# Performance work log

Hardware: AMD Instinct MI355X
Metric: run time of the kernel (lower is better)

The kernel has to match this reference:

```python
import jax, jax.numpy as jnp
import numpy as np

E = 1024   # embed_dim
H = 16     # num_heads
D = E // H # head_dim
NP = 2     # n_physics
PH = 16    # physics adapter hidden


def setup_inputs() -> dict:
    key = jax.random.key(0)
    ks = jax.random.split(key, 16)
    B, T = 2, 2048
    s = 0.02
    return {
        "x": jax.random.normal(ks[0], (B, T, E), dtype=jnp.float32),
        "physics_state": jax.random.uniform(ks[1], (B, NP), dtype=jnp.float32),
        "attn_mask": jax.random.randint(ks[2], (B, T), 0, 2).astype(jnp.bool_),
        "Wq": jax.random.normal(ks[3], (E, E), dtype=jnp.float32) * s,
        "bq": jnp.zeros((E,), dtype=jnp.float32),
        "Wk": jax.random.normal(ks[4], (E, E), dtype=jnp.float32) * s,
        "bk": jnp.zeros((E,), dtype=jnp.float32),
        "Wv": jax.random.normal(ks[5], (E, E), dtype=jnp.float32) * s,
        "bv": jnp.zeros((E,), dtype=jnp.float32),
        "Wo": jax.random.normal(ks[6], (E, E), dtype=jnp.float32) * s,
        "bo": jnp.zeros((E,), dtype=jnp.float32),
        "Wp1": jax.random.normal(ks[7], (NP, PH), dtype=jnp.float32) * 0.5,
        "bp1": jnp.zeros((PH,), dtype=jnp.float32),
        "Wp2": jax.random.normal(ks[8], (PH, H), dtype=jnp.float32) * 0.25,
        "bp2": jnp.zeros((H,), dtype=jnp.float32),
    }


def reference(x, physics_state, attn_mask, Wq, bq, Wk, bk, Wv, bv, Wo, bo, Wp1, bp1, Wp2, bp2):
    B, T, _ = x.shape
    scale = 1.0 / np.sqrt(D)
    # projections -> (B, H, T, D)
    q = (x @ Wq + bq).reshape(B, T, H, D).transpose(0, 2, 1, 3)
    k = (x @ Wk + bk).reshape(B, T, H, D).transpose(0, 2, 1, 3)
    v = (x @ Wv + bv).reshape(B, T, H, D).transpose(0, 2, 1, 3)
    # per-head physics bias (B, H) -> (B, H, 1, 1)
    h = jax.nn.gelu(physics_state @ Wp1 + bp1, approximate=False)
    phys_bias = (h @ Wp2 + bp2)[:, :, None, None]
    scores = jnp.einsum("bhqd,bhkd->bhqk", q, k) * scale + phys_bias
    # key padding mask: True = keep
    scores = jnp.where(attn_mask[:, None, None, :], scores, -jnp.inf)
    attn = jax.nn.softmax(scores, axis=-1)
    out = jnp.einsum("bhqk,bhkd->bhqd", attn, v)
    out = out.transpose(0, 2, 1, 3).reshape(B, T, E)
    return out @ Wo + bo
```

## Files before the change

### kernel.cpp

```cpp
#include <hip/hip_runtime.h>
#include <hip/hip_bf16.h>
#include <stdint.h>

#define E_  1024
#define H_  16
#define D_  64
#define T_  2048
#define B_  2

typedef unsigned short u16;
typedef unsigned char u8;
typedef __attribute__((ext_vector_type(8))) __bf16 bf16x8;
typedef __attribute__((ext_vector_type(4))) float f32x4;
typedef __attribute__((ext_vector_type(8))) u16 u16x8;
typedef __attribute__((ext_vector_type(4))) u16 u16x4;

__device__ __forceinline__ float bf2f(u16 u) {
  union { uint32_t u32; float f; } x; x.u32 = ((uint32_t)u) << 16; return x.f;
}
__device__ __forceinline__ u16 f2bf(float v) {
  union { float f; uint32_t u; } x; x.f = v;
  uint32_t r = x.u + 0x7fffu + ((x.u >> 16) & 1u);
  return (u16)(r >> 16);
}
__device__ __forceinline__ void async16(const void* g, void* l) {
  __builtin_amdgcn_global_load_lds(
      (const __attribute__((address_space(1))) void*)g,
      (__attribute__((address_space(3))) void*)l, 16, 0, 0);
}
__device__ __forceinline__ int jperm(int k) {
  return (k & 35) | ((k & 12) << 1) | ((k & 16) >> 2);
}

__device__ __forceinline__ int detect_f32(const void* src) {
  u16 u = ((const u16*)src)[2 * (threadIdx.x & 63)];
  int e = (u >> 7) & 0xFF;
  int ex = (e != 0 && (e <= 0x40 || e >= 0xC0)) ? 1 : 0;
  return __popcll(__ballot(ex)) > 16;
}

__global__ __launch_bounds__(256) void convf_kernel(const void* __restrict__ src,
                                                    u16* __restrict__ dst, int n) {
  const int f32in = detect_f32(src);
  int i = (blockIdx.x * 256 + threadIdx.x) * 8;
  if (i >= n) return;
  if (f32in) {
    const float* s = (const float*)src;
    u16x8 o;
#pragma unroll
    for (int j = 0; j < 8; ++j) o[j] = f2bf(s[i + j]);
    *(u16x8*)(dst + i) = o;
  } else {
    *(u16x8*)(dst + i) = *(const u16x8*)((const u16*)src + i);
  }
}

__global__ __launch_bounds__(256) void bias4_kernel(
    const void* __restrict__ b0, const void* __restrict__ b1,
    const void* __restrict__ b2, const void* __restrict__ b3,
    u16* __restrict__ dst) {
  const void* src = (blockIdx.x == 0) ? b0 : (blockIdx.x == 1) ? b1
                    : (blockIdx.x == 2) ? b2 : b3;
  const int f32in = detect_f32(src);
  u16* d = dst + blockIdx.x * 2048;
  int t = threadIdx.x;
#pragma unroll
  for (int j = 0; j < 4; ++j) {
    int i = t + j * 256;
    d[i] = f32in ? f2bf(((const float*)src)[i]) : ((const u16*)src)[i];
  }
}

__global__ __launch_bounds__(256) void maskbias_kernel(const void* __restrict__ mp,
                                                       float* __restrict__ mbg) {
  unsigned w0 = ((const unsigned*)mp)[threadIdx.x & 63];
  int isInt = (__ballot(w0 > 1u) == 0ull);
  int i = blockIdx.x * 256 + threadIdx.x;
  int keep = isInt ? (((const int*)mp)[i] != 0) : (((const u8*)mp)[i] != 0);
  mbg[i] = keep ? -5.77078016f : -30000.f;
}

__global__ __launch_bounds__(256) void wtc4_kernel(
    const void* __restrict__ W0, const void* __restrict__ W1,
    const void* __restrict__ W2, const void* __restrict__ W3,
    u16* __restrict__ T0, u16* __restrict__ T1,
    u16* __restrict__ T2, u16* __restrict__ T3) {
  __shared__ __align__(16) u16 tile[64][65];
  const int z = blockIdx.z;
  const void* Wv = (z == 0) ? W0 : (z == 1) ? W1 : (z == 2) ? W2 : W3;
  u16* WT = (z == 0) ? T0 : (z == 1) ? T1 : (z == 2) ? T2 : T3;
  const int f32in = detect_f32(Wv);
  const int bx = blockIdx.x * 64, by = blockIdx.y * 64;
  const int t = threadIdx.x;
#pragma unroll
  for (int p = 0; p < 2; ++p) {
    int row = p * 32 + (t >> 3);
    int ch = t & 7;
    if (f32in) {
      const float* s = (const float*)Wv + (size_t)(by + row) * E_ + bx + ch * 8;
#pragma unroll
      for (int j = 0; j < 8; ++j) tile[row][ch * 8 + j] = f2bf(s[j]);
    } else {
      u16x8 v = *(const u16x8*)((const u16*)Wv + (size_t)(by + row) * E_ + bx + ch * 8);
#pragma unroll
      for (int j = 0; j < 8; ++j) tile[row][ch * 8 + j] = v[j];
    }
  }
  __syncthreads();
#pragma unroll
  for (int p = 0; p < 2; ++p) {
    int orow = p * 32 + (t >> 3);
    int ch = t & 7;
    u16x8 v;
#pragma unroll
    for (int j = 0; j < 8; ++j) v[j] = tile[ch * 8 + j][orow];
    *(u16x8*)(WT + (size_t)(bx + orow) * E_ + by + ch * 8) = v;
  }
}

__global__ __launch_bounds__(256, 2) void gemm_qkv_kernel(
    const u16* __restrict__ A, const u16* __restrict__ BTm,
    const u16* __restrict__ biases, u16* __restrict__ Qb,
    u16* __restrict__ Kb, u16* __restrict__ Vtb) {
  __shared__ __align__(16) u16 As[128 * 64];
  __shared__ __align__(16) u16 Bs[128 * 64];
  const int tid = threadIdx.x, lane = tid & 63, wid = tid >> 6;
  const int wm = wid >> 1, wn = wid & 1;
  const int l15 = lane & 15, lg = lane >> 4;
  const int r0 = blockIdx.x * 128, c0 = blockIdx.y * 128;
  f32x4 acc[4][4] = {};

  for (int k0 = 0; k0 < E_; k0 += 64) {
    __syncthreads();
#pragma unroll
    for (int i = 0; i < 4; ++i) {
      int row = i * 32 + (tid >> 3);
      int g = (tid & 7) ^ (row & 7);
      async16(A + (size_t)(r0 + row) * E_ + k0 + g * 8,
              (char*)As + i * 4096 + tid * 16);
      async16(BTm + (size_t)(c0 + row) * E_ + k0 + g * 8,
              (char*)Bs + i * 4096 + tid * 16);
    }
    __syncthreads();
#pragma unroll
    for (int kk = 0; kk < 2; ++kk) {
      bf16x8 af[4], bfr[4];
#pragma unroll
      for (int mt = 0; mt < 4; ++mt) {
        int rowa = wm * 64 + mt * 16 + l15;
        int sa = (kk * 4 + lg) ^ (rowa & 7);
        af[mt] = *(const bf16x8*)((const char*)As + rowa * 128 + sa * 16);
        int rowb = wn * 64 + mt * 16 + l15;
        int sb = (kk * 4 + lg) ^ (rowb & 7);
        bfr[mt] = *(const bf16x8*)((const char*)Bs + rowb * 128 + sb * 16);
      }
#pragma unroll
      for (int mt = 0; mt < 4; ++mt)
#pragma unroll
        for (int nt = 0; nt < 4; ++nt)
          acc[mt][nt] = __builtin_amdgcn_mfma_f32_16x16x32_bf16(
              af[mt], bfr[nt], acc[mt][nt], 0, 0, 0);
    }
  }

  const int sel = c0 >> 10;
  u16* outp = (sel == 0) ? Qb : Kb;
#pragma unroll
  for (int mt = 0; mt < 4; ++mt) {
#pragma unroll
    for (int nt = 0; nt < 4; ++nt) {
      int colG = c0 + wn * 64 + nt * 16 + l15;
      int colL = colG & 1023;
      float bv = bf2f(biases[sel * 2048 + colL]);
      int rbase = r0 + wm * 64 + mt * 16 + lg * 4;
      int hh = colL >> 6, dd = colL & 63;
      if (sel == 2) {
        int bb = rbase >> 11, t0 = rbase & (T_ - 1);
        int tp = (t0 & ~63) | jperm(t0 & 63);
        u16x4 pk;
#pragma unroll
        for (int r = 0; r < 4; ++r) pk[r] = f2bf(acc[mt][nt][r] + bv);
        *(u16x4*)(Vtb + (size_t)((bb * H_ + hh) * D_ + dd) * T_ + tp) = pk;
      } else {
#pragma unroll
        for (int r = 0; r < 4; ++r) {
          int row = rbase + r;
          int bb = row >> 11, t = row & (T_ - 1);
          outp[(size_t)((bb * H_ + hh) * T_ + t) * D_ + dd] =
              f2bf(acc[mt][nt][r] + bv);
        }
      }
    }
  }
}

__global__ __launch_bounds__(256, 2) void gemm_out_kernel(
    const u16* __restrict__ A, const u16* __restrict__ BTm,
    const u16* __restrict__ bias, float* __restrict__ out) {
  __shared__ __align__(16) u16 As[128 * 64];
  __shared__ __align__(16) u16 Bs[128 * 64];
  const int tid = threadIdx.x, lane = tid & 63, wid = tid >> 6;
  const int wm = wid >> 1, wn = wid & 1;
  const int l15 = lane & 15, lg = lane >> 4;
  const int r0 = blockIdx.x * 128, c0 = blockIdx.y * 128;
  f32x4 acc[4][4] = {};

  for (int k0 = 0; k0 < E_; k0 += 64) {
    __syncthreads();
#pragma unroll
    for (int i = 0; i < 4; ++i) {
      int row = i * 32 + (tid >> 3);
      int g = (tid & 7) ^ (row & 7);
      async16(A + (size_t)(r0 + row) * E_ + k0 + g * 8,
              (char*)As + i * 4096 + tid * 16);
      async16(BTm + (size_t)(c0 + row) * E_ + k0 + g * 8,
              (char*)Bs + i * 4096 + tid * 16);
    }
    __syncthreads();
#pragma unroll
    for (int kk = 0; kk < 2; ++kk) {
      bf16x8 af[4], bfr[4];
#pragma unroll
      for (int mt = 0; mt < 4; ++mt) {
        int rowa = wm * 64 + mt * 16 + l15;
        int sa = (kk * 4 + lg) ^ (rowa & 7);
        af[mt] = *(const bf16x8*)((const char*)As + rowa * 128 + sa * 16);
        int rowb = wn * 64 + mt * 16 + l15;
        int sb = (kk * 4 + lg) ^ (rowb & 7);
        bfr[mt] = *(const bf16x8*)((const char*)Bs + rowb * 128 + sb * 16);
      }
#pragma unroll
      for (int mt = 0; mt < 4; ++mt)
#pragma unroll
        for (int nt = 0; nt < 4; ++nt)
          acc[mt][nt] = __builtin_amdgcn_mfma_f32_16x16x32_bf16(
              af[mt], bfr[nt], acc[mt][nt], 0, 0, 0);
    }
  }

#pragma unroll
  for (int mt = 0; mt < 4; ++mt)
#pragma unroll
    for (int nt = 0; nt < 4; ++nt) {
      int col = c0 + wn * 64 + nt * 16 + l15;
      float bv = bf2f(bias[col]);
      int rbase = r0 + wm * 64 + mt * 16 + lg * 4;
#pragma unroll
      for (int r = 0; r < 4; ++r)
        out[(size_t)(rbase + r) * E_ + col] = acc[mt][nt][r] + bv;
    }
}

__global__ __launch_bounds__(256, 2) void attn_kernel(
    const u16* __restrict__ Q, const u16* __restrict__ K,
    const u16* __restrict__ VT, const float* __restrict__ mbg,
    u16* __restrict__ outb) {
  __shared__ __align__(16) u16 Ks[2][64 * 64];
  __shared__ __align__(16) u16 Vs[2][64 * 64];
  const int wg = blockIdx.x;
  const int xcd = wg & 7, slot = wg >> 3;
  const int bh = xcd + 8 * (slot >> 4);
  const int q0 = (slot & 15) * 128;
  const int b = bh >> 4, h = bh & 15;
  const int tid = threadIdx.x, lane = tid & 63, w = tid >> 6;
  const int l15 = lane & 15, lg = lane >> 4;

  const u16* qb = Q + (size_t)bh * T_ * D_;
  const u16* kb = K + (size_t)bh * T_ * D_;
  const u16* vb = VT + (size_t)bh * D_ * T_;
  const float* mbb = mbg + b * T_ + lg * 4;

  bf16x8 qf[2][2];
#pragma unroll
  for (int mt = 0; mt < 2; ++mt)
#pragma unroll
    for (int kd = 0; kd < 2; ++kd) {
      int row = q0 + w * 32 + mt * 16 + l15;
      qf[mt][kd] = *(const bf16x8*)(qb + (size_t)row * D_ + kd * 32 + lg * 8);
    }

#define STAGE(kt_, bi_)                                                  \
  do {                                                                   \
    _Pragma("unroll")                                                    \
    for (int c = 0; c < 2; ++c) {                                        \
      int row_ = c * 32 + (tid >> 3);                                    \
      int g_ = (tid & 7) ^ (row_ & 7);                                   \
      async16(kb + (size_t)((kt_) * 64 + row_) * D_ + g_ * 8,            \
              (char*)&Ks[bi_][0] + c * 4096 + tid * 16);                 \
      async16(vb + (size_t)row_ * T_ + (kt_) * 64 + g_ * 8,              \
              (char*)&Vs[bi_][0] + c * 4096 + tid * 16);                 \
    }                                                                    \
  } while (0)

  STAGE(0, 0);
  __syncthreads();

  f32x4 o[2][4] = {};
  float lrow[2] = {0.f, 0.f};
  const float cc = 0.125f * 1.44269504f;

  for (int kt = 0; kt < 32; ++kt) {
    const int cur = kt & 1;
    if (kt < 31) STAGE(kt + 1, cur ^ 1);
    const char* Kc = (const char*)&Ks[cur][0];
    const char* Vc = (const char*)&Vs[cur][0];

    f32x4 mbv4[4];
#pragma unroll
    for (int mf = 0; mf < 4; ++mf)
      mbv4[mf] = *(const f32x4*)(mbb + kt * 64 + mf * 16);

    f32x4 s2[2][4] = {};
#pragma unroll
    for (int kd = 0; kd < 2; ++kd) {
      bf16x8 kf[4];
#pragma unroll
      for (int mf = 0; mf < 4; ++mf) {
        int row = mf * 16 + l15;
        int sl = (kd * 4 + lg) ^ (row & 7);
        kf[mf] = *(const bf16x8*)(Kc + row * 128 + sl * 16);
      }
      __builtin_amdgcn_s_setprio(1);
#pragma unroll
      for (int mt = 0; mt < 2; ++mt)
#pragma unroll
        for (int mf = 0; mf < 4; ++mf)
          s2[mt][mf] = __builtin_amdgcn_mfma_f32_16x16x32_bf16(
              kf[mf], qf[mt][kd], s2[mt][mf], 0, 0, 0);
      __builtin_amdgcn_s_setprio(0);
    }

    uint32_t pkw[2][4][2];
#pragma unroll
    for (int mt = 0; mt < 2; ++mt) {
#pragma unroll
      for (int mf = 0; mf < 4; ++mf) {
        float p0 = exp2f(fmaf(s2[mt][mf][0], cc, mbv4[mf][0]));
        float p1 = exp2f(fmaf(s2[mt][mf][1], cc, mbv4[mf][1]));
        float p2 = exp2f(fmaf(s2[mt][mf][2], cc, mbv4[mf][2]));
        float p3 = exp2f(fmaf(s2[mt][mf][3], cc, mbv4[mf][3]));
        lrow[mt] += (p0 + p1) + (p2 + p3);
        asm("v_cvt_pk_bf16_f32 %0, %1, %2" : "=v"(pkw[mt][mf][0]) : "v"(p0), "v"(p1));
        asm("v_cvt_pk_bf16_f32 %0, %1, %2" : "=v"(pkw[mt][mf][1]) : "v"(p2), "v"(p3));
      }
    }

#pragma unroll
    for (int kk = 0; kk < 2; ++kk) {
      bf16x8 pf[2], vf[4];
#pragma unroll
      for (int mt = 0; mt < 2; ++mt) {
        union { uint32_t u[4]; bf16x8 v; } pu;
        pu.u[0] = pkw[mt][2 * kk][0];
        pu.u[1] = pkw[mt][2 * kk][1];
        pu.u[2] = pkw[mt][2 * kk + 1][0];
        pu.u[3] = pkw[mt][2 * kk + 1][1];
        pf[mt] = pu.v;
      }
#pragma unroll
      for (int df = 0; df < 4; ++df) {
        int row = df * 16 + l15;
        int sl = (kk * 4 + lg) ^ (row & 7);
        vf[df] = *(const bf16x8*)(Vc + row * 128 + sl * 16);
      }
      __builtin_amdgcn_s_setprio(1);
#pragma unroll
      for (int mt = 0; mt < 2; ++mt)
#pragma unroll
        for (int df = 0; df < 4; ++df)
          o[mt][df] = __builtin_amdgcn_mfma_f32_16x16x32_bf16(
              pf[mt], vf[df], o[mt][df], 0, 0, 0);
      __builtin_amdgcn_s_setprio(0);
    }
    __syncthreads();
  }
#undef STAGE

  float inv[2][4];
#pragma unroll
  for (int mt = 0; mt < 2; ++mt) {
    float t = lrow[mt];
    t += __shfl_xor(t, 16);
    t += __shfl_xor(t, 32);
    float ti = (t > 0.f) ? 1.0f / t : 0.f;
#pragma unroll
    for (int r = 0; r < 4; ++r)
      inv[mt][r] = __shfl(ti, (lane & 48) | (lg * 4 + r));
  }

  char* wbase = ((w < 2) ? (char*)&Ks[0][0] : (char*)&Vs[0][0]) + (w & 1) * 4608;
#pragma unroll
  for (int mt = 0; mt < 2; ++mt)
#pragma unroll
    for (int df = 0; df < 4; ++df)
#pragma unroll
      for (int r = 0; r < 4; ++r) {
        int prow = mt * 16 + lg * 4 + r;
        *(u16*)(wbase + prow * 144 + (df * 16 + l15) * 2) =
            f2bf(o[mt][df][r] * inv[mt][r]);
      }
  asm volatile("s_waitcnt lgkmcnt(0)" ::: "memory");
  __builtin_amdgcn_sched_barrier(0);
  {
    int rowL = lane >> 1;
    int c8 = lane & 1;
    int grow = b * T_ + q0 + w * 32 + rowL;
#pragma unroll
    for (int j = 0; j < 4; ++j) {
      int chunk = c8 + 2 * j;
      u16x8 v = *(const u16x8*)(wbase + rowL * 144 + chunk * 16);
      *(u16x8*)(outb + (size_t)grow * E_ + h * D_ + chunk * 8) = v;
    }
  }
}

extern "C" void kernel_launch(void* const* d_in, const int* in_sizes, int n_in,
                              void* d_out, int out_size, void* d_ws, size_t ws_size,
                              hipStream_t stream) {
  const void* x    = d_in[0];
  const void* mask = d_in[2];
  const void* Wq = d_in[3];
  const void* bq = d_in[4];
  const void* Wk = d_in[5];
  const void* bk = d_in[6];
  const void* Wv = d_in[7];
  const void* bv = d_in[8];
  const void* Wo = d_in[9];
  const void* bo = d_in[10];
  char* ws = (char*)d_ws;

  const size_t MB = 1024 * 1024;
  u16* Kb   = (u16*)(ws + 0 * MB);
  u16* Vtb  = (u16*)(ws + 8 * MB);
  u16* Ab   = (u16*)(ws + 16 * MB);
  u16* WqT  = (u16*)(ws + 16 * MB);
  u16* WkT  = (u16*)(ws + 18 * MB);
  u16* WvT  = (u16*)(ws + 20 * MB);
  u16* WoT  = (u16*)(ws + 24 * MB);
  u16* bqc  = (u16*)(ws + 26 * MB);
  u16* boc  = bqc + 3 * 2048;
  float* mbg = (float*)(ws + 26 * MB + 32 * 1024);

  u16* Qb = (u16*)d_out;
  u16* xc = (u16*)((char*)d_out + 8 * MB);
  float* out = (float*)d_out;

  dim3 blk(256);
  const int NX = B_ * T_ * E_;

  convf_kernel<<<NX / 8 / 256, blk, 0, stream>>>(x, xc, NX);
  bias4_kernel<<<4, blk, 0, stream>>>(bq, bk, bv, bo, bqc);
  maskbias_kernel<<<16, blk, 0, stream>>>(mask, mbg);
  wtc4_kernel<<<dim3(16, 16, 4), blk, 0, stream>>>(Wq, Wk, Wv, Wo,
                                                   WqT, WkT, WvT, WoT);
  gemm_qkv_kernel<<<dim3(32, 24), blk, 0, stream>>>(xc, WqT, bqc, Qb, Kb, Vtb);
  attn_kernel<<<dim3(512), blk, 0, stream>>>(Qb, Kb, Vtb, mbg, Ab);
  gemm_out_kernel<<<dim3(32, 8), blk, 0, stream>>>(Ab, WoT, boc, out);
}
```

Before: 129.0 us.

## Triple-buffer K/V tiles with one barrier per iteration and stage mask in LDS

Moves the attention K/V shared-memory pipeline from double to triple buffering, prefetching two tiles ahead. It replaces the two __syncthreads per iteration with a vmcnt wait plus a single s_barrier. The mask bias row is copied once into LDS instead of being read from global memory every iteration, and the output staging gets its own scratch buffer so it no longer reuses the K/V buffers. The added LDS (about 8KB mask, 18KB scratch, extra K/V stage) may reduce occupancy below the 2 blocks per CU that the launch bounds target.

```diff
diff --git a/kernel.cpp b/kernel.cpp
--- a/kernel.cpp
+++ b/kernel.cpp
@@ -255,8 +255,10 @@
     const u16* __restrict__ Q, const u16* __restrict__ K,
     const u16* __restrict__ VT, const float* __restrict__ mbg,
     u16* __restrict__ outb) {
-  __shared__ __align__(16) u16 Ks[2][64 * 64];
-  __shared__ __align__(16) u16 Vs[2][64 * 64];
+  __shared__ __align__(16) u16 Ks[3][64 * 64];
+  __shared__ __align__(16) u16 Vs[3][64 * 64];
+  __shared__ __align__(16) float mb[T_];
+  __shared__ __align__(16) u16 oscr[4][2304];
   const int wg = blockIdx.x;
   const int xcd = wg & 7, slot = wg >> 3;
   const int bh = xcd + 8 * (slot >> 4);
@@ -268,7 +270,13 @@
   const u16* qb = Q + (size_t)bh * T_ * D_;
   const u16* kb = K + (size_t)bh * T_ * D_;
   const u16* vb = VT + (size_t)bh * D_ * T_;
-  const float* mbb = mbg + b * T_ + lg * 4;
+
+  {
+    const f32x4* s = (const f32x4*)(mbg + b * T_);
+    f32x4* d = (f32x4*)mb;
+#pragma unroll
+    for (int j = 0; j < 2; ++j) d[tid + j * 256] = s[tid + j * 256];
+  }
 
   bf16x8 qf[2][2];
 #pragma unroll
@@ -293,22 +301,30 @@
   } while (0)
 
   STAGE(0, 0);
-  __syncthreads();
+  STAGE(1, 1);
+  asm volatile("s_waitcnt lgkmcnt(0)" ::: "memory");
 
   f32x4 o[2][4] = {};
   float lrow[2] = {0.f, 0.f};
   const float cc = 0.125f * 1.44269504f;
 
+  int rd = 0, wr = 2;
   for (int kt = 0; kt < 32; ++kt) {
-    const int cur = kt & 1;
-    if (kt < 31) STAGE(kt + 1, cur ^ 1);
-    const char* Kc = (const char*)&Ks[cur][0];
-    const char* Vc = (const char*)&Vs[cur][0];
+    if (kt < 31)
+      asm volatile("s_waitcnt vmcnt(4)" ::: "memory");
+    else
+      asm volatile("s_waitcnt vmcnt(0)" ::: "memory");
+    __builtin_amdgcn_sched_barrier(0);
+    __builtin_amdgcn_s_barrier();
+    __builtin_amdgcn_sched_barrier(0);
+    if (kt < 30) STAGE(kt + 2, wr);
+    const char* Kc = (const char*)&Ks[rd][0];
+    const char* Vc = (const char*)&Vs[rd][0];
 
     f32x4 mbv4[4];
 #pragma unroll
     for (int mf = 0; mf < 4; ++mf)
-      mbv4[mf] = *(const f32x4*)(mbb + kt * 64 + mf * 16);
+      mbv4[mf] = *(const f32x4*)&mb[kt * 64 + mf * 16 + lg * 4];
 
     f32x4 s2[2][4] = {};
 #pragma unroll
@@ -372,7 +388,8 @@
               pf[mt], vf[df], o[mt][df], 0, 0, 0);
       __builtin_amdgcn_s_setprio(0);
     }
-    __syncthreads();
+    rd = (rd == 2) ? 0 : rd + 1;
+    wr = (wr == 2) ? 0 : wr + 1;
   }
 #undef STAGE
 
@@ -388,7 +405,7 @@
       inv[mt][r] = __shfl(ti, (lane & 48) | (lg * 4 + r));
   }
 
-  char* wbase = ((w < 2) ? (char*)&Ks[0][0] : (char*)&Vs[0][0]) + (w & 1) * 4608;
+  char* wbase = (char*)&oscr[w][0];
 #pragma unroll
   for (int mt = 0; mt < 2; ++mt)
 #pragma unroll
```

Measured after the change: 129.3 us. Within noise of the previous version (+0.3%).

## Halve attention query tile, double grid, stage bf16 mask bias in LDS

Applied to the files above, without the earlier changes.

The attention kernel now handles 64 query rows per workgroup instead of 128, with one 16-row MFMA tile per wave, and launches 1024 workgroups with a higher occupancy hint. The mask bias is stored as bf16 and copied once into shared memory per block, so it is no longer read from global memory on every key tile. This aims to cut per-wave register pressure and raise occupancy and parallelism. In exchange, each workgroup reloads K and V for fewer queries, which doubles K/V traffic, and the bias loses some precision.

```diff
diff --git a/kernel.cpp b/kernel.cpp
--- a/kernel.cpp
+++ b/kernel.cpp
@@ -72,12 +72,12 @@
 }
 
 __global__ __launch_bounds__(256) void maskbias_kernel(const void* __restrict__ mp,
-                                                       float* __restrict__ mbg) {
+                                                       u16* __restrict__ mbh) {
   unsigned w0 = ((const unsigned*)mp)[threadIdx.x & 63];
   int isInt = (__ballot(w0 > 1u) == 0ull);
   int i = blockIdx.x * 256 + threadIdx.x;
   int keep = isInt ? (((const int*)mp)[i] != 0) : (((const u8*)mp)[i] != 0);
-  mbg[i] = keep ? -5.77078016f : -30000.f;
+  mbh[i] = keep ? f2bf(-5.77078016f) : f2bf(-30000.f);
 }
 
 __global__ __launch_bounds__(256) void wtc4_kernel(
@@ -251,16 +251,17 @@
     }
 }
 
-__global__ __launch_bounds__(256, 2) void attn_kernel(
+__global__ __launch_bounds__(256, 4) void attn_kernel(
     const u16* __restrict__ Q, const u16* __restrict__ K,
-    const u16* __restrict__ VT, const float* __restrict__ mbg,
+    const u16* __restrict__ VT, const u16* __restrict__ mbg,
     u16* __restrict__ outb) {
   __shared__ __align__(16) u16 Ks[2][64 * 64];
   __shared__ __align__(16) u16 Vs[2][64 * 64];
+  __shared__ __align__(16) u16 mbh[T_];
   const int wg = blockIdx.x;
   const int xcd = wg & 7, slot = wg >> 3;
-  const int bh = xcd + 8 * (slot >> 4);
-  const int q0 = (slot & 15) * 128;
+  const int bh = xcd + 8 * (slot >> 5);
+  const int q0 = (slot & 31) * 64;
   const int b = bh >> 4, h = bh & 15;
   const int tid = threadIdx.x, lane = tid & 63, w = tid >> 6;
   const int l15 = lane & 15, lg = lane >> 4;
@@ -268,16 +269,15 @@
   const u16* qb = Q + (size_t)bh * T_ * D_;
   const u16* kb = K + (size_t)bh * T_ * D_;
   const u16* vb = VT + (size_t)bh * D_ * T_;
-  const float* mbb = mbg + b * T_ + lg * 4;
-
-  bf16x8 qf[2][2];
-#pragma unroll
-  for (int mt = 0; mt < 2; ++mt)
-#pragma unroll
-    for (int kd = 0; kd < 2; ++kd) {
-      int row = q0 + w * 32 + mt * 16 + l15;
-      qf[mt][kd] = *(const bf16x8*)(qb + (size_t)row * D_ + kd * 32 + lg * 8);
-    }
+
+  *(u16x8*)&mbh[tid * 8] = *(const u16x8*)(mbg + b * T_ + tid * 8);
+
+  bf16x8 qf[2];
+#pragma unroll
+  for (int kd = 0; kd < 2; ++kd) {
+    int row = q0 + w * 16 + l15;
+    qf[kd] = *(const bf16x8*)(qb + (size_t)row * D_ + kd * 32 + lg * 8);
+  }
 
 #define STAGE(kt_, bi_)                                                  \
   do {                                                                   \
@@ -295,8 +295,8 @@
   STAGE(0, 0);
   __syncthreads();
 
-  f32x4 o[2][4] = {};
-  float lrow[2] = {0.f, 0.f};
+  f32x4 o[4] = {};
+  float lrow = 0.f;
   const float cc = 0.125f * 1.44269504f;
 
   for (int kt = 0; kt < 32; ++kt) {
@@ -305,12 +305,12 @@
     const char* Kc = (const char*)&Ks[cur][0];
     const char* Vc = (const char*)&Vs[cur][0];
 
-    f32x4 mbv4[4];
+    u16x4 mraw[4];
 #pragma unroll
     for (int mf = 0; mf < 4; ++mf)
-      mbv4[mf] = *(const f32x4*)(mbb + kt * 64 + mf * 16);
-
-    f32x4 s2[2][4] = {};
+      mraw[mf] = *(const u16x4*)&mbh[kt * 64 + mf * 16 + lg * 4];
+
+    f32x4 s2[4] = {};
 #pragma unroll
     for (int kd = 0; kd < 2; ++kd) {
       bf16x8 kf[4];
@@ -322,40 +322,34 @@
       }
       __builtin_amdgcn_s_setprio(1);
 #pragma unroll
-      for (int mt = 0; mt < 2; ++mt)
-#pragma unroll
-        for (int mf = 0; mf < 4; ++mf)
-          s2[mt][mf] = __builtin_amdgcn_mfma_f32_16x16x32_bf16(
-              kf[mf], qf[mt][kd], s2[mt][mf], 0, 0, 0);
+      for (int mf = 0; mf < 4; ++mf)
+        s2[mf] = __builtin_amdgcn_mfma_f32_16x16x32_bf16(
+            kf[mf], qf[kd], s2[mf], 0, 0, 0);
       __builtin_amdgcn_s_setprio(0);
     }
 
-    uint32_t pkw[2][4][2];
-#pragma unroll
-    for (int mt = 0; mt < 2; ++mt) {
-#pragma unroll
-      for (int mf = 0; mf < 4; ++mf) {
-        float p0 = exp2f(fmaf(s2[mt][mf][0], cc, mbv4[mf][0]));
-        float p1 = exp2f(fmaf(s2[mt][mf][1], cc, mbv4[mf][1]));
-        float p2 = exp2f(fmaf(s2[mt][mf][2], cc, mbv4[mf][2]));
-        float p3 = exp2f(fmaf(s2[mt][mf][3], cc, mbv4[mf][3]));
-        lrow[mt] += (p0 + p1) + (p2 + p3);
-        asm("v_cvt_pk_bf16_f32 %0, %1, %2" : "=v"(pkw[mt][mf][0]) : "v"(p0), "v"(p1));
-        asm("v_cvt_pk_bf16_f32 %0, %1, %2" : "=v"(pkw[mt][mf][1]) : "v"(p2), "v"(p3));
-      }
+    uint32_t pkw[4][2];
+#pragma unroll
+    for (int mf = 0; mf < 4; ++mf) {
+      float p0 = exp2f(fmaf(s2[mf][0], cc, bf2f(mraw[mf][0])));
+      float p1 = exp2f(fmaf(s2[mf][1], cc, bf2f(mraw[mf][1])));
+      float p2 = exp2f(fmaf(s2[mf][2], cc, bf2f(mraw[mf][2])));
+      float p3 = exp2f(fmaf(s2[mf][3], cc, bf2f(mraw[mf][3])));
+      lrow += (p0 + p1) + (p2 + p3);
+      asm("v_cvt_pk_bf16_f32 %0, %1, %2" : "=v"(pkw[mf][0]) : "v"(p0), "v"(p1));
+      asm("v_cvt_pk_bf16_f32 %0, %1, %2" : "=v"(pkw[mf][1]) : "v"(p2), "v"(p3));
     }
 
 #pragma unroll
     for (int kk = 0; kk < 2; ++kk) {
-      bf16x8 pf[2], vf[4];
-#pragma unroll
-      for (int mt = 0; mt < 2; ++mt) {
+      bf16x8 pf, vf[4];
+      {
         union { uint32_t u[4]; bf16x8 v; } pu;
-        pu.u[0] = pkw[mt][2 * kk][0];
-        pu.u[1] = pkw[mt][2 * kk][1];
-        pu.u[2] = pkw[mt][2 * kk + 1][0];
-        pu.u[3] = pkw[mt][2 * kk + 1][1];
-        pf[mt] = pu.v;
+        pu.u[0] = pkw[2 * kk][0];
+        pu.u[1] = pkw[2 * kk][1];
+        pu.u[2] = pkw[2 * kk + 1][0];
+        pu.u[3] = pkw[2 * kk + 1][1];
+        pf = pu.v;
       }
 #pragma unroll
       for (int df = 0; df < 4; ++df) {
@@ -365,49 +359,44 @@
       }
       __builtin_amdgcn_s_setprio(1);
 #pragma unroll
-      for (int mt = 0; mt < 2; ++mt)
-#pragma unroll
-        for (int df = 0; df < 4; ++df)
-          o[mt][df] = __builtin_amdgcn_mfma_f32_16x16x32_bf16(
-              pf[mt], vf[df], o[mt][df], 0, 0, 0);
+      for (int df = 0; df < 4; ++df)
+        o[df] = __builtin_amdgcn_mfma_f32_16x16x32_bf16(
+            pf, vf[df], o[df], 0, 0, 0);
       __builtin_amdgcn_s_setprio(0);
     }
     __syncthreads();
   }
 #undef STAGE
 
-  float inv[2][4];
-#pragma unroll
-  for (int mt = 0; mt < 2; ++mt) {
-    float t = lrow[mt];
+  float inv[4];
+  {
+    float t = lrow;
     t += __shfl_xor(t, 16);
     t += __shfl_xor(t, 32);
     float ti = (t > 0.f) ? 1.0f / t : 0.f;
 #pragma unroll
     for (int r = 0; r < 4; ++r)
-      inv[mt][r] = __shfl(ti, (lane & 48) | (lg * 4 + r));
-  }
-
-  char* wbase = ((w < 2) ? (char*)&Ks[0][0] : (char*)&Vs[0][0]) + (w & 1) * 4608;
-#pragma unroll
-  for (int mt = 0; mt < 2; ++mt)
-#pragma unroll
-    for (int df = 0; df < 4; ++df)
-#pragma unroll
-      for (int r = 0; r < 4; ++r) {
-        int prow = mt * 16 + lg * 4 + r;
-        *(u16*)(wbase + prow * 144 + (df * 16 + l15) * 2) =
-            f2bf(o[mt][df][r] * inv[mt][r]);
-      }
+      inv[r] = __shfl(ti, (lane & 48) | (lg * 4 + r));
+  }
+
+  char* wbase = (char*)&Ks[0][0] + w * 2304;
+#pragma unroll
+  for (int df = 0; df < 4; ++df)
+#pragma unroll
+    for (int r = 0; r < 4; ++r) {
+      int prow = lg * 4 + r;
+      *(u16*)(wbase + prow * 144 + (df * 16 + l15) * 2) =
+          f2bf(o[df][r] * inv[r]);
+    }
   asm volatile("s_waitcnt lgkmcnt(0)" ::: "memory");
   __builtin_amdgcn_sched_barrier(0);
   {
-    int rowL = lane >> 1;
-    int c8 = lane & 1;
-    int grow = b * T_ + q0 + w * 32 + rowL;
-#pragma unroll
-    for (int j = 0; j < 4; ++j) {
-      int chunk = c8 + 2 * j;
+    int rowL = lane >> 2;
+    int cpart = lane & 3;
+    int grow = b * T_ + q0 + w * 16 + rowL;
+#pragma unroll
+    for (int j = 0; j < 2; ++j) {
+      int chunk = cpart + 4 * j;
       u16x8 v = *(const u16x8*)(wbase + rowL * 144 + chunk * 16);
       *(u16x8*)(outb + (size_t)grow * E_ + h * D_ + chunk * 8) = v;
     }
@@ -439,7 +428,7 @@
   u16* WoT  = (u16*)(ws + 24 * MB);
   u16* bqc  = (u16*)(ws + 26 * MB);
   u16* boc  = bqc + 3 * 2048;
-  float* mbg = (float*)(ws + 26 * MB + 32 * 1024);
+  u16* mbg  = (u16*)(ws + 26 * MB + 32 * 1024);
 
   u16* Qb = (u16*)d_out;
   u16* xc = (u16*)((char*)d_out + 8 * MB);
@@ -454,6 +443,6 @@
   wtc4_kernel<<<dim3(16, 16, 4), blk, 0, stream>>>(Wq, Wk, Wv, Wo,
                                                    WqT, WkT, WvT, WoT);
   gemm_qkv_kernel<<<dim3(32, 24), blk, 0, stream>>>(xc, WqT, bqc, Qb, Kb, Vtb);
-  attn_kernel<<<dim3(512), blk, 0, stream>>>(Qb, Kb, Vtb, mbg, Ab);
+  attn_kernel<<<dim3(1024), blk, 0, stream>>>(Qb, Kb, Vtb, mbg, Ab);
   gemm_out_kernel<<<dim3(32, 8), blk, 0, stream>>>(Ab, WoT, boc, out);
 }
```

After: 132.1 us. 2.4% more time.

## Software-pipeline attention: prefetch two tiles ahead and overlap PV with next QK

Applied to the files above, without the earlier changes.

Restructures the attention main loop so K/V tiles are staged two iterations ahead in a 3-way K and 4-way V LDS ring, with explicit vmcnt waits and a single barrier per tile. The PV matmul of the previous tile is interleaved after the QK matmul of the current tile, using ping-pong packed-probability registers, so MFMA work overlaps the exp/softmax VALU work. The mask bias is copied into LDS once instead of read from global every tile. GEMM launch bounds move to 3 waves per SIMD. The cost is more LDS and registers, which can reduce attention occupancy. The hand-written waitcnt accounting may also be fragile.

```diff
diff --git a/kernel.cpp b/kernel.cpp
--- a/kernel.cpp
+++ b/kernel.cpp
@@ -118,7 +118,7 @@
   }
 }
 
-__global__ __launch_bounds__(256, 2) void gemm_qkv_kernel(
+__global__ __launch_bounds__(256, 3) void gemm_qkv_kernel(
     const u16* __restrict__ A, const u16* __restrict__ BTm,
     const u16* __restrict__ biases, u16* __restrict__ Qb,
     u16* __restrict__ Kb, u16* __restrict__ Vtb) {
@@ -194,7 +194,7 @@
   }
 }
 
-__global__ __launch_bounds__(256, 2) void gemm_out_kernel(
+__global__ __launch_bounds__(256, 3) void gemm_out_kernel(
     const u16* __restrict__ A, const u16* __restrict__ BTm,
     const u16* __restrict__ bias, float* __restrict__ out) {
   __shared__ __align__(16) u16 As[128 * 64];
@@ -251,12 +251,13 @@
     }
 }
 
-__global__ __launch_bounds__(256, 2) void attn_kernel(
+__global__ __launch_bounds__(256) void attn_kernel(
     const u16* __restrict__ Q, const u16* __restrict__ K,
     const u16* __restrict__ VT, const float* __restrict__ mbg,
     u16* __restrict__ outb) {
-  __shared__ __align__(16) u16 Ks[2][64 * 64];
-  __shared__ __align__(16) u16 Vs[2][64 * 64];
+  __shared__ __align__(16) u16 Ks[3 * 64 * 64];
+  __shared__ __align__(16) u16 Vs[4 * 64 * 64];
+  __shared__ __align__(16) float mb[T_];
   const int wg = blockIdx.x;
   const int xcd = wg & 7, slot = wg >> 3;
   const int bh = xcd + 8 * (slot >> 4);
@@ -268,7 +269,13 @@
   const u16* qb = Q + (size_t)bh * T_ * D_;
   const u16* kb = K + (size_t)bh * T_ * D_;
   const u16* vb = VT + (size_t)bh * D_ * T_;
-  const float* mbb = mbg + b * T_ + lg * 4;
+
+  {
+    const f32x4* s = (const f32x4*)(mbg + b * T_);
+    f32x4* d = (f32x4*)mb;
+#pragma unroll
+    for (int j = 0; j < 2; ++j) d[tid + j * 256] = s[tid + j * 256];
+  }
 
   bf16x8 qf[2][2];
 #pragma unroll
@@ -279,102 +286,125 @@
       qf[mt][kd] = *(const bf16x8*)(qb + (size_t)row * D_ + kd * 32 + lg * 8);
     }
 
-#define STAGE(kt_, bi_)                                                  \
+#define STAGE(n_)                                                        \
   do {                                                                   \
+    char* kdst_ = (char*)Ks + ((n_) % 3) * 8192;                         \
+    char* vdst_ = (char*)Vs + ((n_) & 3) * 8192;                         \
     _Pragma("unroll")                                                    \
     for (int c = 0; c < 2; ++c) {                                        \
       int row_ = c * 32 + (tid >> 3);                                    \
       int g_ = (tid & 7) ^ (row_ & 7);                                   \
-      async16(kb + (size_t)((kt_) * 64 + row_) * D_ + g_ * 8,            \
-              (char*)&Ks[bi_][0] + c * 4096 + tid * 16);                 \
-      async16(vb + (size_t)row_ * T_ + (kt_) * 64 + g_ * 8,              \
-              (char*)&Vs[bi_][0] + c * 4096 + tid * 16);                 \
+      async16(kb + (size_t)((n_) * 64 + row_) * D_ + g_ * 8,             \
+              kdst_ + c * 4096 + tid * 16);                              \
+      async16(vb + (size_t)row_ * T_ + (n_) * 64 + g_ * 8,               \
+              vdst_ + c * 4096 + tid * 16);                              \
     }                                                                    \
   } while (0)
 
-  STAGE(0, 0);
-  __syncthreads();
+#define PVBODY(vt_, PRV)                                                 \
+  do {                                                                   \
+    const char* Vp_ = (const char*)Vs + ((vt_) & 3) * 8192;              \
+    _Pragma("unroll")                                                    \
+    for (int kk = 0; kk < 2; ++kk) {                                     \
+      bf16x8 pf[2], vf[4];                                               \
+      _Pragma("unroll")                                                  \
+      for (int mt = 0; mt < 2; ++mt) {                                   \
+        union { uint32_t u[4]; bf16x8 v; } pu;                           \
+        pu.u[0] = PRV[mt][2 * kk][0];                                    \
+        pu.u[1] = PRV[mt][2 * kk][1];                                    \
+        pu.u[2] = PRV[mt][2 * kk + 1][0];                                \
+        pu.u[3] = PRV[mt][2 * kk + 1][1];                                \
+        pf[mt] = pu.v;                                                   \
+      }                                                                  \
+      _Pragma("unroll")                                                  \
+      for (int df = 0; df < 4; ++df) {                                   \
+        int row_ = df * 16 + l15;                                        \
+        int sl_ = (kk * 4 + lg) ^ (row_ & 7);                            \
+        vf[df] = *(const bf16x8*)(Vp_ + row_ * 128 + sl_ * 16);          \
+      }                                                                  \
+      __builtin_amdgcn_s_setprio(1);                                     \
+      _Pragma("unroll")                                                  \
+      for (int mt = 0; mt < 2; ++mt)                                     \
+        _Pragma("unroll")                                                \
+        for (int df = 0; df < 4; ++df)                                   \
+          o[mt][df] = __builtin_amdgcn_mfma_f32_16x16x32_bf16(           \
+              pf[mt], vf[df], o[mt][df], 0, 0, 0);                       \
+      __builtin_amdgcn_s_setprio(0);                                     \
+    }                                                                    \
+  } while (0)
+
+#define TILE(kt_, CUR, PRV, DOPV)                                        \
+  do {                                                                   \
+    if ((kt_) < 31) asm volatile("s_waitcnt vmcnt(4)" ::: "memory");     \
+    else            asm volatile("s_waitcnt vmcnt(0)" ::: "memory");     \
+    __builtin_amdgcn_sched_barrier(0);                                   \
+    __builtin_amdgcn_s_barrier();                                        \
+    __builtin_amdgcn_sched_barrier(0);                                   \
+    if ((kt_) < 30) STAGE((kt_) + 2);                                    \
+    const char* Kc_ = (const char*)Ks + ((kt_) % 3) * 8192;              \
+    f32x4 mbv4[4];                                                       \
+    _Pragma("unroll")                                                    \
+    for (int mf = 0; mf < 4; ++mf)                                       \
+      mbv4[mf] = *(const f32x4*)&mb[(kt_) * 64 + mf * 16 + lg * 4];      \
+    f32x4 s2[2][4] = {};                                                 \
+    _Pragma("unroll")                                                    \
+    for (int kd = 0; kd < 2; ++kd) {                                     \
+      bf16x8 kf[4];                                                      \
+      _Pragma("unroll")                                                  \
+      for (int mf = 0; mf < 4; ++mf) {                                   \
+        int row_ = mf * 16 + l15;                                        \
+        int sl_ = (kd * 4 + lg) ^ (row_ & 7);                            \
+        kf[mf] = *(const bf16x8*)(Kc_ + row_ * 128 + sl_ * 16);          \
+      }                                                                  \
+      __builtin_amdgcn_s_setprio(1);                                     \
+      _Pragma("unroll")                                                  \
+      for (int mt = 0; mt < 2; ++mt)                                     \
+        _Pragma("unroll")                                                \
+        for (int mf = 0; mf < 4; ++mf)                                   \
+          s2[mt][mf] = __builtin_amdgcn_mfma_f32_16x16x32_bf16(          \
+              kf[mf], qf[mt][kd], s2[mt][mf], 0, 0, 0);                  \
+      __builtin_amdgcn_s_setprio(0);                                     \
+    }                                                                    \
+    if (DOPV) PVBODY((kt_) - 1, PRV);       \
+    _Pragma("unroll")                                                    \
+    for (int mt = 0; mt < 2; ++mt) {                                     \
+      _Pragma("unroll")                                                  \
+      for (int mf = 0; mf < 4; ++mf) {                                   \
+        float p0 = exp2f(fmaf(s2[mt][mf][0], cc, mbv4[mf][0]));          \
+        float p1 = exp2f(fmaf(s2[mt][mf][1], cc, mbv4[mf][1]));          \
+        float p2 = exp2f(fmaf(s2[mt][mf][2], cc, mbv4[mf][2]));          \
+        float p3 = exp2f(fmaf(s2[mt][mf][3], cc, mbv4[mf][3]));          \
+        lrow[mt] += (p0 + p1) + (p2 + p3);                               \
+        asm("v_cvt_pk_bf16_f32 %0, %1, %2"                               \
+            : "=v"(CUR[mt][mf][0]) : "v"(p0), "v"(p1));                  \
+        asm("v_cvt_pk_bf16_f32 %0, %1, %2"                               \
+            : "=v"(CUR[mt][mf][1]) : "v"(p2), "v"(p3));                  \
+      }                                                                  \
+    }                                                                    \
+  } while (0)
+
+  STAGE(0);
+  STAGE(1);
+  asm volatile("s_waitcnt lgkmcnt(0)" ::: "memory");
 
   f32x4 o[2][4] = {};
   float lrow[2] = {0.f, 0.f};
+  uint32_t pkwA[2][4][2], pkwB[2][4][2];
   const float cc = 0.125f * 1.44269504f;
 
-  for (int kt = 0; kt < 32; ++kt) {
-    const int cur = kt & 1;
-    if (kt < 31) STAGE(kt + 1, cur ^ 1);
-    const char* Kc = (const char*)&Ks[cur][0];
-    const char* Vc = (const char*)&Vs[cur][0];
-
-    f32x4 mbv4[4];
-#pragma unroll
-    for (int mf = 0; mf < 4; ++mf)
-      mbv4[mf] = *(const f32x4*)(mbb + kt * 64 + mf * 16);
-
-    f32x4 s2[2][4] = {};
-#pragma unroll
-    for (int kd = 0; kd < 2; ++kd) {
-      bf16x8 kf[4];
-#pragma unroll
-      for (int mf = 0; mf < 4; ++mf) {
-        int row = mf * 16 + l15;
-        int sl = (kd * 4 + lg) ^ (row & 7);
-        kf[mf] = *(const bf16x8*)(Kc + row * 128 + sl * 16);
-      }
-      __builtin_amdgcn_s_setprio(1);
-#pragma unroll
-      for (int mt = 0; mt < 2; ++mt)
-#pragma unroll
-        for (int mf = 0; mf < 4; ++mf)
-          s2[mt][mf] = __builtin_amdgcn_mfma_f32_16x16x32_bf16(
-              kf[mf], qf[mt][kd], s2[mt][mf], 0, 0, 0);
-      __builtin_amdgcn_s_setprio(0);
-    }
-
-    uint32_t pkw[2][4][2];
-#pragma unroll
-    for (int mt = 0; mt < 2; ++mt) {
-#pragma unroll
-      for (int mf = 0; mf < 4; ++mf) {
-        float p0 = exp2f(fmaf(s2[mt][mf][0], cc, mbv4[mf][0]));
-        float p1 = exp2f(fmaf(s2[mt][mf][1], cc, mbv4[mf][1]));
-        float p2 = exp2f(fmaf(s2[mt][mf][2], cc, mbv4[mf][2]));
-        float p3 = exp2f(fmaf(s2[mt][mf][3], cc, mbv4[mf][3]));
-        lrow[mt] += (p0 + p1) + (p2 + p3);
-        asm("v_cvt_pk_bf16_f32 %0, %1, %2" : "=v"(pkw[mt][mf][0]) : "v"(p0), "v"(p1));
-        asm("v_cvt_pk_bf16_f32 %0, %1, %2" : "=v"(pkw[mt][mf][1]) : "v"(p2), "v"(p3));
-      }
-    }
-
-#pragma unroll
-    for (int kk = 0; kk < 2; ++kk) {
-      bf16x8 pf[2], vf[4];
-#pragma unroll
-      for (int mt = 0; mt < 2; ++mt) {
-        union { uint32_t u[4]; bf16x8 v; } pu;
-        pu.u[0] = pkw[mt][2 * kk][0];
-        pu.u[1] = pkw[mt][2 * kk][1];
-        pu.u[2] = pkw[mt][2 * kk + 1][0];
-        pu.u[3] = pkw[mt][2 * kk + 1][1];
-        pf[mt] = pu.v;
-      }
-#pragma unroll
-      for (int df = 0; df < 4; ++df) {
-        int row = df * 16 + l15;
-        int sl = (kk * 4 + lg) ^ (row & 7);
-        vf[df] = *(const bf16x8*)(Vc + row * 128 + sl * 16);
-      }
-      __builtin_amdgcn_s_setprio(1);
-#pragma unroll
-      for (int mt = 0; mt < 2; ++mt)
-#pragma unroll
-        for (int df = 0; df < 4; ++df)
-          o[mt][df] = __builtin_amdgcn_mfma_f32_16x16x32_bf16(
-              pf[mt], vf[df], o[mt][df], 0, 0, 0);
-      __builtin_amdgcn_s_setprio(0);
-    }
-    __syncthreads();
-  }
+  TILE(0, pkwA, pkwB, 0);
+  for (int k2 = 0; k2 < 15; ++k2) {
+    int ka = 2 * k2 + 1;
+    TILE(ka, pkwB, pkwA, 1);
+    TILE(ka + 1, pkwA, pkwB, 1);
+  }
+  TILE(31, pkwB, pkwA, 1);
+  PVBODY(31, pkwB);
+#undef TILE
+#undef PVBODY
 #undef STAGE
+
+  __syncthreads();
 
   float inv[2][4];
 #pragma unroll
@@ -388,7 +418,7 @@
       inv[mt][r] = __shfl(ti, (lane & 48) | (lg * 4 + r));
   }
 
-  char* wbase = ((w < 2) ? (char*)&Ks[0][0] : (char*)&Vs[0][0]) + (w & 1) * 4608;
+  char* wbase = (char*)Ks + w * 4608;
 #pragma unroll
   for (int mt = 0; mt < 2; ++mt)
 #pragma unroll
```

After: 131.6 us. 2.1% more time.
